# Performance work log

Measured on AMD Instinct MI355X. Metric: run time of the kernel, lower is better.

Reference implementation:

```python
import jax, jax.numpy as jnp
import numpy as np

GRID_LON = 17  # idx = lat*17 + lon in original code


def setup_inputs() -> dict:
    key = jax.random.key(0)
    ks = jax.random.split(key, 16)
    B, S, L = 512, 256, 64
    DIM_RHO, DIM_C, HID = 256, 128, 512
    N_LAT, N_LON = 17, GRID_LON

    rho = jax.random.normal(ks[0], (B, S, DIM_RHO), dtype=jnp.float32)
    c = jax.random.normal(ks[1], (1, DIM_C, N_LAT, N_LON), dtype=jnp.float32)
    w = jax.random.uniform(ks[2], (B, S), dtype=jnp.float32, minval=1e-3, maxval=1.0)
    l = jax.random.uniform(ks[3], (B,), dtype=jnp.float32, minval=0.1, maxval=10.0)
    roads = jax.random.randint(ks[4], (B, L), 0, N_LAT * N_LON)
    lon_idx = jax.random.randint(ks[5], (B, L), 0, N_LON)
    lat_idx = jax.random.randint(ks[6], (B, L), 0, N_LAT)

    sc = lambda fan_in: 1.0 / np.sqrt(fan_in)
    # f2: MLP(128, 256, 128) with selu
    f2_W1 = jax.random.uniform(ks[7], (DIM_C, 256), jnp.float32, -sc(DIM_C), sc(DIM_C))
    f2_b1 = jnp.zeros((256,), jnp.float32)
    f2_W2 = jax.random.uniform(ks[8], (256, DIM_C), jnp.float32, -sc(256), sc(256))
    f2_b2 = jnp.zeros((DIM_C,), jnp.float32)
    # f: MLP2(dim_rho + dim_c, hidden, 1) with selu (use_selu=True)
    fin = DIM_RHO + DIM_C
    f_W1 = jax.random.uniform(ks[9], (fin, HID), jnp.float32, -sc(fin), sc(fin))
    f_b1 = jnp.zeros((HID,), jnp.float32)
    f_W21 = jax.random.uniform(ks[10], (HID, 1), jnp.float32, -sc(HID), sc(HID))
    f_b21 = jnp.zeros((1,), jnp.float32)
    f_W22 = jax.random.uniform(ks[11], (HID, 1), jnp.float32, -sc(HID), sc(HID))
    f_b22 = jnp.zeros((1,), jnp.float32)

    return dict(rho=rho, c=c, w=w, l=l, roads=roads, lon_idx=lon_idx,
                lat_idx=lat_idx, f2_W1=f2_W1, f2_b1=f2_b1, f2_W2=f2_W2,
                f2_b2=f2_b2, f_W1=f_W1, f_b1=f_b1, f_W21=f_W21, f_b21=f_b21,
                f_W22=f_W22, f_b22=f_b22)


def reference(rho, c, w, l, roads, lon_idx, lat_idx,
              f2_W1, f2_b1, f2_W2, f2_b2,
              f_W1, f_b1, f_W21, f_b21, f_W22, f_b22):
    # c: (1, dim_c, n_lat, n_lon) -> (n_lat*n_lon, dim_c)
    c3 = jnp.squeeze(c, 0)                       # (dim_c, n_lat, n_lon)
    c_flat = jnp.transpose(c3, (1, 2, 0)).reshape(-1, c3.shape[0])  # (cells, dim_c)

    # ragged gather-mean, vectorized: (B, L) cell indices -> (B, dim_c)
    idx = lat_idx * GRID_LON + lon_idx           # (B, L)
    c_traj = jnp.mean(c_flat[idx], axis=1)       # (B, dim_c)

    # f2: selu MLP (dropout inactive / eval mode)
    h = jax.nn.selu(c_traj @ f2_W1 + f2_b1)
    c_tr = h @ f2_W2 + f2_b2                     # (B, dim_c)

    # broadcast over seq and concat with rho
    S = rho.shape[1]
    c_exp = jnp.broadcast_to(c_tr[:, None, :], (rho.shape[0], S, c_tr.shape[-1]))
    x = jnp.concatenate([rho, c_exp], axis=2)    # (B, S, dim_rho + dim_c)

    # f (MLP2, selu since use_selu=True)
    h1 = jax.nn.selu(x @ f_W1 + f_b1)            # (B, S, hidden)
    logm = (h1 @ f_W21 + f_b21)[..., 0]          # (B, S)
    logv = (h1 @ f_W22 + f_b22)[..., 0]          # (B, S)

    logw = jnp.log(w)
    logm_agg = jax.nn.logsumexp(logm + logw, axis=1)       # (B,)
    logv_agg = jax.nn.logsumexp(logv + 2.0 * logw, axis=1) # (B,)
    logl = jnp.log(l)
    log_mu = logl - logm_agg
    log_lambda = logl - 3.0 * logm_agg - logv_agg
    return (log_mu, log_lambda)
```

## Files before the change

### kernel.cpp

```cpp
#include <hip/hip_runtime.h>
#include <hip/hip_bf16.h>

typedef short bf16x8 __attribute__((ext_vector_type(8)));
typedef float f32x4 __attribute__((ext_vector_type(4)));
typedef _Float16 half4 __attribute__((ext_vector_type(4)));

__device__ __forceinline__ short f2bf(float f) {
    union { float f; unsigned u; } v; v.f = f;
    unsigned r = (v.u + 0x7FFFu + ((v.u >> 16) & 1u)) >> 16;
    return (short)r;
}

__device__ __forceinline__ float selu_f(float x) {
    const float scale = 1.0507009873554805f;
    const float sa = 1.0507009873554805f * 1.6732632423543772f;
    return x > 0.f ? scale * x : sa * (__expf(x) - 1.f);
}

__global__ void __launch_bounds__(512) prep_all_kernel(
    const float* __restrict__ c, const int* __restrict__ lat_idx,
    const int* __restrict__ lon_idx,
    const float* __restrict__ f2W1, const float* __restrict__ f2b1,
    const float* __restrict__ f2W2, const float* __restrict__ f2b2,
    const float* __restrict__ fW1, const float* __restrict__ fb1,
    const float* __restrict__ fW21, const float* __restrict__ fW22,
    short* __restrict__ w1img, _Float16* __restrict__ wvec,
    float* __restrict__ cbias)
{
    const int bid = blockIdx.x;
    const int t = threadIdx.x;

    if (bid < 512) {
        __shared__ int cells[64];
        __shared__ float ctraj[128];
        __shared__ float hbuf[256];
        __shared__ float ctrf[128];
        const int b = bid;

        if (t < 64) cells[t] = lat_idx[b * 64 + t] * 17 + lon_idx[b * 64 + t];
        __syncthreads();

        if (t < 128) {
            float s = 0.f;
            #pragma unroll 8
            for (int j = 0; j < 64; ++j) s += c[t * 289 + cells[j]];
            ctraj[t] = s * (1.f / 64.f);
        }
        __syncthreads();

        if (t < 256) {
            float acc = f2b1[t];
            #pragma unroll 8
            for (int i = 0; i < 128; ++i) acc += ctraj[i] * f2W1[i * 256 + t];
            hbuf[t] = selu_f(acc);
        }
        __syncthreads();

        if (t < 128) {
            float acc = f2b2[t];
            #pragma unroll 8
            for (int i = 0; i < 256; ++i) acc += hbuf[i] * f2W2[i * 128 + t];
            ctrf[t] = acc;
        }
        __syncthreads();

        float acc = fb1[t];
        #pragma unroll 8
        for (int i = 0; i < 128; ++i) acc += ctrf[i] * fW1[(256 + i) * 512 + t];
        cbias[b * 512 + t] = acc;
    } else if (bid < 768) {
        int I = (bid - 512) * 512 + t;
        int e = I & 7;
        int lane = (I >> 3) & 63;
        int cg = (I >> 9) & 31;
        int kc = I >> 14;
        int col = cg * 16 + (lane & 15);
        int k = kc * 32 + ((lane >> 4) << 3) + e;
        w1img[I] = f2bf(fW1[k * 512 + col]);
    } else {
        int I = (bid - 768) * 512 + t;
        int e = I & 3;
        int lane = (I >> 2) & 63;
        int nc = I >> 8;
        int l15 = lane & 15, hi = lane >> 4;
        int n = nc * 16 + hi * 4 + e;
        float v = (l15 == 0) ? fW21[n] : (l15 == 1 ? fW22[n] : 0.f);
        wvec[I] = (_Float16)v;
    }
}

__global__ void __launch_bounds__(512, 4) fused_gemm_kernel(
    const float* __restrict__ rho, const short* __restrict__ w1img,
    const float* __restrict__ cbias, const _Float16* __restrict__ wvec,
    float* __restrict__ plmP, float* __restrict__ plvP)
{
    __shared__ __align__(16) char smA[36864];

    const int tid  = threadIdx.x;
    const int lane = tid & 63;
    const int w    = tid >> 6;
    const int l15  = lane & 15;
    const int hi   = lane >> 4;

    const int b  = blockIdx.x >> 3;
    const int s0 = ((blockIdx.x >> 1) & 3) << 6;
    const int nh = blockIdx.x & 1;

    const char* bp = (const char*)w1img + (nh * 16 + w * 2) * 1024 + lane * 16;
    bf16x8 bAll[16];
    #pragma unroll
    for (int j = 0; j < 16; ++j)
        bAll[j] = *(const bf16x8*)(bp + (size_t)(j >> 1) * 32768 + (j & 1) * 1024);

    {
        const float* src = rho + (size_t)(b * 256 + s0) * 256 + tid * 8;
        float4 fa[8];
        #pragma unroll
        for (int j = 0; j < 4; ++j) {
            fa[2 * j]     = *(const float4*)(src + j * 4096);
            fa[2 * j + 1] = *(const float4*)(src + j * 4096 + 4);
        }
        const int kc_w = (tid >> 2) & 7;
        const int hi_w = tid & 3;
        const int sw_w = (tid >> 5) ^ (tid & 15);
        #pragma unroll
        for (int j = 0; j < 4; ++j) {
            union { bf16x8 h; unsigned u[4]; } pk;
            asm("v_cvt_pk_bf16_f32 %0, %1, %2" : "=v"(pk.u[0]) : "v"(fa[2*j].x), "v"(fa[2*j].y));
            asm("v_cvt_pk_bf16_f32 %0, %1, %2" : "=v"(pk.u[1]) : "v"(fa[2*j].z), "v"(fa[2*j].w));
            asm("v_cvt_pk_bf16_f32 %0, %1, %2" : "=v"(pk.u[2]) : "v"(fa[2*j+1].x), "v"(fa[2*j+1].y));
            asm("v_cvt_pk_bf16_f32 %0, %1, %2" : "=v"(pk.u[3]) : "v"(fa[2*j+1].z), "v"(fa[2*j+1].w));
            int slot = (kc_w * 4 + j) * 64 + hi_w * 16 + sw_w;
            *(bf16x8*)(smA + (slot << 4)) = pk.h;
        }
    }
    __syncthreads();

    f32x4 acc[2][4];
    #pragma unroll
    for (int nf = 0; nf < 2; ++nf)
        #pragma unroll
        for (int sf = 0; sf < 4; ++sf)
            acc[nf][sf] = (f32x4){0.f, 0.f, 0.f, 0.f};

    #pragma unroll
    for (int kc = 0; kc < 8; ++kc) {
        const int sw_r = l15 ^ (((kc & 3) << 2) | hi);
        const char* ab = smA + ((kc * 256 + hi * 16 + sw_r) << 4);
        bf16x8 aF[4];
        #pragma unroll
        for (int sf = 0; sf < 4; ++sf)
            aF[sf] = *(const bf16x8*)(ab + sf * 1024);
        #pragma unroll
        for (int nf = 0; nf < 2; ++nf)
            #pragma unroll
            for (int sf = 0; sf < 4; ++sf)
                acc[nf][sf] = __builtin_amdgcn_mfma_f32_16x16x32_bf16(
                    bAll[kc * 2 + nf], aF[sf], acc[nf][sf], 0, 0, 0);
    }

    f32x4 rd[4];
    #pragma unroll
    for (int sf = 0; sf < 4; ++sf) rd[sf] = (f32x4){0.f, 0.f, 0.f, 0.f};

    #pragma unroll
    for (int nf = 0; nf < 2; ++nf) {
        const int nc = nh * 16 + w * 2 + nf;
        f32x4 cbf = *(const f32x4*)(cbias + b * 512 + nc * 16 + hi * 4);
        half4 wv = *(const half4*)(wvec + (size_t)nc * 256 + lane * 4);
        #pragma unroll
        for (int sf = 0; sf < 4; ++sf) {
            half4 pa;
            #pragma unroll
            for (int q = 0; q < 4; ++q)
                pa[q] = (_Float16)selu_f(acc[nf][sf][q] + cbf[q]);
            rd[sf] = __builtin_amdgcn_mfma_f32_16x16x16f16(pa, wv, rd[sf], 0, 0, 0);
        }
    }

    float* redM = (float*)(smA + 32768);
    float* redV = (float*)(smA + 34816);
    if (l15 == 0) {
        #pragma unroll
        for (int sf = 0; sf < 4; ++sf)
            *(f32x4*)&redM[w * 64 + sf * 16 + hi * 4] = rd[sf];
    } else if (l15 == 1) {
        #pragma unroll
        for (int sf = 0; sf < 4; ++sf)
            *(f32x4*)&redV[w * 64 + sf * 16 + hi * 4] = rd[sf];
    }

    __syncthreads();
    size_t obase = (size_t)nh * 131072 + (size_t)b * 256 + s0;
    if (tid < 64) {
        float s = 0.f;
        #pragma unroll
        for (int j = 0; j < 8; ++j) s += redM[j * 64 + tid];
        plmP[obase + tid] = s;
    } else if (tid < 128) {
        int rr = tid - 64;
        float s = 0.f;
        #pragma unroll
        for (int j = 0; j < 8; ++j) s += redV[j * 64 + rr];
        plvP[obase + rr] = s;
    }
}

__global__ void __launch_bounds__(64) finalize_kernel(
    const float* __restrict__ plmP, const float* __restrict__ plvP,
    const float* __restrict__ w, const float* __restrict__ l,
    const float* __restrict__ b21p, const float* __restrict__ b22p,
    float* __restrict__ out)
{
    const int b = blockIdx.x;
    const int lane = threadIdx.x;
    const float b21 = b21p[0], b22 = b22p[0];

    float a1[4], a2[4];
    float m1 = -1e30f, m2 = -1e30f;
    #pragma unroll
    for (int i = 0; i < 4; ++i) {
        int s = i * 64 + lane;
        int idx = b * 256 + s;
        float lw = logf(w[idx]);
        a1[i] = plmP[idx] + plmP[131072 + idx] + b21 + lw;
        a2[i] = plvP[idx] + plvP[131072 + idx] + b22 + 2.f * lw;
        m1 = fmaxf(m1, a1[i]);
        m2 = fmaxf(m2, a2[i]);
    }
    #pragma unroll
    for (int m = 1; m < 64; m <<= 1) {
        m1 = fmaxf(m1, __shfl_xor(m1, m));
        m2 = fmaxf(m2, __shfl_xor(m2, m));
    }
    float s1 = 0.f, s2 = 0.f;
    #pragma unroll
    for (int i = 0; i < 4; ++i) {
        s1 += expf(a1[i] - m1);
        s2 += expf(a2[i] - m2);
    }
    #pragma unroll
    for (int m = 1; m < 64; m <<= 1) {
        s1 += __shfl_xor(s1, m);
        s2 += __shfl_xor(s2, m);
    }
    if (lane == 0) {
        float lm_agg = m1 + logf(s1);
        float lv_agg = m2 + logf(s2);
        float logl = logf(l[b]);
        out[b]       = logl - lm_agg;
        out[512 + b] = logl - 3.f * lm_agg - lv_agg;
    }
}

extern "C" void kernel_launch(void* const* d_in, const int* in_sizes, int n_in,
                              void* d_out, int out_size, void* d_ws, size_t ws_size,
                              hipStream_t stream) {
    const float* rho     = (const float*)d_in[0];
    const float* c       = (const float*)d_in[1];
    const float* w       = (const float*)d_in[2];
    const float* l       = (const float*)d_in[3];
    const int*   lon_idx = (const int*)d_in[5];
    const int*   lat_idx = (const int*)d_in[6];
    const float* f2W1    = (const float*)d_in[7];
    const float* f2b1    = (const float*)d_in[8];
    const float* f2W2    = (const float*)d_in[9];
    const float* f2b2    = (const float*)d_in[10];
    const float* fW1     = (const float*)d_in[11];
    const float* fb1     = (const float*)d_in[12];
    const float* fW21    = (const float*)d_in[13];
    const float* fb21    = (const float*)d_in[14];
    const float* fW22    = (const float*)d_in[15];
    const float* fb22    = (const float*)d_in[16];
    float* out = (float*)d_out;

    char* ws = (char*)d_ws;
    float*     cbias = (float*)(ws);
    short*     w1img = (short*)(ws + 1048576);
    float*     plmP  = (float*)(ws + 1310720);
    float*     plvP  = (float*)(ws + 2359296);
    _Float16*  wvec  = (_Float16*)(ws + 3407872);

    prep_all_kernel<<<784, 512, 0, stream>>>(c, lat_idx, lon_idx,
                                             f2W1, f2b1, f2W2, f2b2,
                                             fW1, fb1, fW21, fW22,
                                             w1img, wvec, cbias);
    fused_gemm_kernel<<<4096, 512, 0, stream>>>(rho, w1img, cbias, wvec,
                                                plmP, plvP);
    finalize_kernel<<<512, 64, 0, stream>>>(plmP, plvP, w, l, fb21, fb22, out);
}
```

Measured before the change: 98.66 us.

## Make GEMM blocks persistent over four seq tiles with double-buffered rho staging

Each block now handles all four 64-row sequence tiles for one batch and one N-half, so the grid shrinks from 4096 to 1024 blocks. The bf16 weight fragments are loaded once and reused across the tiles. The next tile's rho loads are issued before the current tile's MFMA work and converted into a second LDS buffer, overlapping global loads with compute. In exchange, LDS use roughly doubles to 68KB, which can lower occupancy, there are fewer blocks to spread across CUs, and register pressure rises from holding the prefetched data.

```diff
diff --git a/kernel.cpp b/kernel.cpp
--- a/kernel.cpp
+++ b/kernel.cpp
@@ -94,7 +94,7 @@
     const float* __restrict__ cbias, const _Float16* __restrict__ wvec,
     float* __restrict__ plmP, float* __restrict__ plvP)
 {
-    __shared__ __align__(16) char smA[36864];
+    __shared__ __align__(16) char smem[69632];
 
     const int tid  = threadIdx.x;
     const int lane = tid & 63;
@@ -102,9 +102,9 @@
     const int l15  = lane & 15;
     const int hi   = lane >> 4;
 
-    const int b  = blockIdx.x >> 3;
-    const int s0 = ((blockIdx.x >> 1) & 3) << 6;
-    const int nh = blockIdx.x & 1;
+    const int bid = blockIdx.x;
+    const int nh  = (bid >> 3) & 1;
+    const int b   = ((bid >> 4) << 3) | (bid & 7);
 
     const char* bp = (const char*)w1img + (nh * 16 + w * 2) * 1024 + lane * 16;
     bf16x8 bAll[16];
@@ -112,97 +112,158 @@
     for (int j = 0; j < 16; ++j)
         bAll[j] = *(const bf16x8*)(bp + (size_t)(j >> 1) * 32768 + (j & 1) * 1024);
 
+    const int kc_w = (tid >> 2) & 7;
+    const int hi_w = tid & 3;
+    const int sw_w = (tid >> 5) ^ (tid & 15);
+    const float* srcB = rho + (size_t)(b * 256) * 256 + tid * 8;
+
+    float* redM = (float*)(smem + 65536);
+    float* redV = (float*)(smem + 67584);
+
     {
-        const float* src = rho + (size_t)(b * 256 + s0) * 256 + tid * 8;
-        float4 fa[8];
         #pragma unroll
         for (int j = 0; j < 4; ++j) {
-            fa[2 * j]     = *(const float4*)(src + j * 4096);
-            fa[2 * j + 1] = *(const float4*)(src + j * 4096 + 4);
-        }
-        const int kc_w = (tid >> 2) & 7;
-        const int hi_w = tid & 3;
-        const int sw_w = (tid >> 5) ^ (tid & 15);
-        #pragma unroll
-        for (int j = 0; j < 4; ++j) {
+            float4 f0 = *(const float4*)(srcB + j * 4096);
+            float4 f1 = *(const float4*)(srcB + j * 4096 + 4);
             union { bf16x8 h; unsigned u[4]; } pk;
-            asm("v_cvt_pk_bf16_f32 %0, %1, %2" : "=v"(pk.u[0]) : "v"(fa[2*j].x), "v"(fa[2*j].y));
-            asm("v_cvt_pk_bf16_f32 %0, %1, %2" : "=v"(pk.u[1]) : "v"(fa[2*j].z), "v"(fa[2*j].w));
-            asm("v_cvt_pk_bf16_f32 %0, %1, %2" : "=v"(pk.u[2]) : "v"(fa[2*j+1].x), "v"(fa[2*j+1].y));
-            asm("v_cvt_pk_bf16_f32 %0, %1, %2" : "=v"(pk.u[3]) : "v"(fa[2*j+1].z), "v"(fa[2*j+1].w));
+            asm("v_cvt_pk_bf16_f32 %0, %1, %2" : "=v"(pk.u[0]) : "v"(f0.x), "v"(f0.y));
+            asm("v_cvt_pk_bf16_f32 %0, %1, %2" : "=v"(pk.u[1]) : "v"(f0.z), "v"(f0.w));
+            asm("v_cvt_pk_bf16_f32 %0, %1, %2" : "=v"(pk.u[2]) : "v"(f1.x), "v"(f1.y));
+            asm("v_cvt_pk_bf16_f32 %0, %1, %2" : "=v"(pk.u[3]) : "v"(f1.z), "v"(f1.w));
             int slot = (kc_w * 4 + j) * 64 + hi_w * 16 + sw_w;
-            *(bf16x8*)(smA + (slot << 4)) = pk.h;
+            *(bf16x8*)(smem + (slot << 4)) = pk.h;
         }
     }
     __syncthreads();
 
-    f32x4 acc[2][4];
-    #pragma unroll
-    for (int nf = 0; nf < 2; ++nf)
-        #pragma unroll
-        for (int sf = 0; sf < 4; ++sf)
-            acc[nf][sf] = (f32x4){0.f, 0.f, 0.f, 0.f};
-
-    #pragma unroll
-    for (int kc = 0; kc < 8; ++kc) {
-        const int sw_r = l15 ^ (((kc & 3) << 2) | hi);
-        const char* ab = smA + ((kc * 256 + hi * 16 + sw_r) << 4);
-        bf16x8 aF[4];
-        #pragma unroll
-        for (int sf = 0; sf < 4; ++sf)
-            aF[sf] = *(const bf16x8*)(ab + sf * 1024);
+    #pragma unroll
+    for (int st = 0; st < 4; ++st) {
+        char* bufC = smem + (st & 1) * 32768;
+        char* bufN = smem + ((st + 1) & 1) * 32768;
+        const float* srcN = srcB + (st + 1) * 16384;
+
+        float4 fa0, fa1, fa2, fa3;
+        if (st < 3) {
+            fa0 = *(const float4*)(srcN);
+            fa1 = *(const float4*)(srcN + 4);
+            fa2 = *(const float4*)(srcN + 4096);
+            fa3 = *(const float4*)(srcN + 4096 + 4);
+        }
+
+        f32x4 acc[2][4];
         #pragma unroll
         for (int nf = 0; nf < 2; ++nf)
             #pragma unroll
             for (int sf = 0; sf < 4; ++sf)
-                acc[nf][sf] = __builtin_amdgcn_mfma_f32_16x16x32_bf16(
-                    bAll[kc * 2 + nf], aF[sf], acc[nf][sf], 0, 0, 0);
-    }
-
-    f32x4 rd[4];
-    #pragma unroll
-    for (int sf = 0; sf < 4; ++sf) rd[sf] = (f32x4){0.f, 0.f, 0.f, 0.f};
-
-    #pragma unroll
-    for (int nf = 0; nf < 2; ++nf) {
-        const int nc = nh * 16 + w * 2 + nf;
-        f32x4 cbf = *(const f32x4*)(cbias + b * 512 + nc * 16 + hi * 4);
-        half4 wv = *(const half4*)(wvec + (size_t)nc * 256 + lane * 4);
-        #pragma unroll
-        for (int sf = 0; sf < 4; ++sf) {
-            half4 pa;
-            #pragma unroll
-            for (int q = 0; q < 4; ++q)
-                pa[q] = (_Float16)selu_f(acc[nf][sf][q] + cbf[q]);
-            rd[sf] = __builtin_amdgcn_mfma_f32_16x16x16f16(pa, wv, rd[sf], 0, 0, 0);
-        }
-    }
-
-    float* redM = (float*)(smA + 32768);
-    float* redV = (float*)(smA + 34816);
-    if (l15 == 0) {
-        #pragma unroll
-        for (int sf = 0; sf < 4; ++sf)
-            *(f32x4*)&redM[w * 64 + sf * 16 + hi * 4] = rd[sf];
-    } else if (l15 == 1) {
-        #pragma unroll
-        for (int sf = 0; sf < 4; ++sf)
-            *(f32x4*)&redV[w * 64 + sf * 16 + hi * 4] = rd[sf];
-    }
-
-    __syncthreads();
-    size_t obase = (size_t)nh * 131072 + (size_t)b * 256 + s0;
-    if (tid < 64) {
-        float s = 0.f;
-        #pragma unroll
-        for (int j = 0; j < 8; ++j) s += redM[j * 64 + tid];
-        plmP[obase + tid] = s;
-    } else if (tid < 128) {
-        int rr = tid - 64;
-        float s = 0.f;
-        #pragma unroll
-        for (int j = 0; j < 8; ++j) s += redV[j * 64 + rr];
-        plvP[obase + rr] = s;
+                acc[nf][sf] = (f32x4){0.f, 0.f, 0.f, 0.f};
+
+        #pragma unroll
+        for (int kc = 0; kc < 8; ++kc) {
+            const int sw_r = l15 ^ (((kc & 3) << 2) | hi);
+            const char* ab = bufC + ((kc * 256 + hi * 16 + sw_r) << 4);
+            bf16x8 aF[4];
+            #pragma unroll
+            for (int sf = 0; sf < 4; ++sf)
+                aF[sf] = *(const bf16x8*)(ab + sf * 1024);
+            #pragma unroll
+            for (int nf = 0; nf < 2; ++nf)
+                #pragma unroll
+                for (int sf = 0; sf < 4; ++sf)
+                    acc[nf][sf] = __builtin_amdgcn_mfma_f32_16x16x32_bf16(
+                        bAll[kc * 2 + nf], aF[sf], acc[nf][sf], 0, 0, 0);
+        }
+
+        float4 fb0, fb1v, fb2, fb3;
+        if (st < 3) {
+            {
+                union { bf16x8 h; unsigned u[4]; } pk;
+                asm("v_cvt_pk_bf16_f32 %0, %1, %2" : "=v"(pk.u[0]) : "v"(fa0.x), "v"(fa0.y));
+                asm("v_cvt_pk_bf16_f32 %0, %1, %2" : "=v"(pk.u[1]) : "v"(fa0.z), "v"(fa0.w));
+                asm("v_cvt_pk_bf16_f32 %0, %1, %2" : "=v"(pk.u[2]) : "v"(fa1.x), "v"(fa1.y));
+                asm("v_cvt_pk_bf16_f32 %0, %1, %2" : "=v"(pk.u[3]) : "v"(fa1.z), "v"(fa1.w));
+                int slot = (kc_w * 4 + 0) * 64 + hi_w * 16 + sw_w;
+                *(bf16x8*)(bufN + (slot << 4)) = pk.h;
+            }
+            {
+                union { bf16x8 h; unsigned u[4]; } pk;
+                asm("v_cvt_pk_bf16_f32 %0, %1, %2" : "=v"(pk.u[0]) : "v"(fa2.x), "v"(fa2.y));
+                asm("v_cvt_pk_bf16_f32 %0, %1, %2" : "=v"(pk.u[1]) : "v"(fa2.z), "v"(fa2.w));
+                asm("v_cvt_pk_bf16_f32 %0, %1, %2" : "=v"(pk.u[2]) : "v"(fa3.x), "v"(fa3.y));
+                asm("v_cvt_pk_bf16_f32 %0, %1, %2" : "=v"(pk.u[3]) : "v"(fa3.z), "v"(fa3.w));
+                int slot = (kc_w * 4 + 1) * 64 + hi_w * 16 + sw_w;
+                *(bf16x8*)(bufN + (slot << 4)) = pk.h;
+            }
+            fb0  = *(const float4*)(srcN + 2 * 4096);
+            fb1v = *(const float4*)(srcN + 2 * 4096 + 4);
+            fb2  = *(const float4*)(srcN + 3 * 4096);
+            fb3  = *(const float4*)(srcN + 3 * 4096 + 4);
+        }
+
+        f32x4 rd[4];
+        #pragma unroll
+        for (int sf = 0; sf < 4; ++sf) rd[sf] = (f32x4){0.f, 0.f, 0.f, 0.f};
+
+        #pragma unroll
+        for (int nf = 0; nf < 2; ++nf) {
+            const int nc = nh * 16 + w * 2 + nf;
+            f32x4 cbf = *(const f32x4*)(cbias + b * 512 + nc * 16 + hi * 4);
+            half4 wv = *(const half4*)(wvec + (size_t)nc * 256 + lane * 4);
+            #pragma unroll
+            for (int sf = 0; sf < 4; ++sf) {
+                half4 pa;
+                #pragma unroll
+                for (int q = 0; q < 4; ++q)
+                    pa[q] = (_Float16)selu_f(acc[nf][sf][q] + cbf[q]);
+                rd[sf] = __builtin_amdgcn_mfma_f32_16x16x16f16(pa, wv, rd[sf], 0, 0, 0);
+            }
+        }
+
+        if (l15 == 0) {
+            #pragma unroll
+            for (int sf = 0; sf < 4; ++sf)
+                *(f32x4*)&redM[w * 64 + sf * 16 + hi * 4] = rd[sf];
+        } else if (l15 == 1) {
+            #pragma unroll
+            for (int sf = 0; sf < 4; ++sf)
+                *(f32x4*)&redV[w * 64 + sf * 16 + hi * 4] = rd[sf];
+        }
+
+        __syncthreads();
+
+        size_t obase = (size_t)nh * 131072 + (size_t)b * 256 + st * 64;
+        if (tid < 64) {
+            float s = 0.f;
+            #pragma unroll
+            for (int j = 0; j < 8; ++j) s += redM[j * 64 + tid];
+            plmP[obase + tid] = s;
+        } else if (tid < 128) {
+            int rr = tid - 64;
+            float s = 0.f;
+            #pragma unroll
+            for (int j = 0; j < 8; ++j) s += redV[j * 64 + rr];
+            plvP[obase + rr] = s;
+        }
+        if (st < 3) {
+            {
+                union { bf16x8 h; unsigned u[4]; } pk;
+                asm("v_cvt_pk_bf16_f32 %0, %1, %2" : "=v"(pk.u[0]) : "v"(fb0.x), "v"(fb0.y));
+                asm("v_cvt_pk_bf16_f32 %0, %1, %2" : "=v"(pk.u[1]) : "v"(fb0.z), "v"(fb0.w));
+                asm("v_cvt_pk_bf16_f32 %0, %1, %2" : "=v"(pk.u[2]) : "v"(fb1v.x), "v"(fb1v.y));
+                asm("v_cvt_pk_bf16_f32 %0, %1, %2" : "=v"(pk.u[3]) : "v"(fb1v.z), "v"(fb1v.w));
+                int slot = (kc_w * 4 + 2) * 64 + hi_w * 16 + sw_w;
+                *(bf16x8*)(bufN + (slot << 4)) = pk.h;
+            }
+            {
+                union { bf16x8 h; unsigned u[4]; } pk;
+                asm("v_cvt_pk_bf16_f32 %0, %1, %2" : "=v"(pk.u[0]) : "v"(fb2.x), "v"(fb2.y));
+                asm("v_cvt_pk_bf16_f32 %0, %1, %2" : "=v"(pk.u[1]) : "v"(fb2.z), "v"(fb2.w));
+                asm("v_cvt_pk_bf16_f32 %0, %1, %2" : "=v"(pk.u[2]) : "v"(fb3.x), "v"(fb3.y));
+                asm("v_cvt_pk_bf16_f32 %0, %1, %2" : "=v"(pk.u[3]) : "v"(fb3.z), "v"(fb3.w));
+                int slot = (kc_w * 4 + 3) * 64 + hi_w * 16 + sw_w;
+                *(bf16x8*)(bufN + (slot << 4)) = pk.h;
+            }
+        }
+        __syncthreads();
     }
 }
 
@@ -285,7 +346,7 @@
                                              f2W1, f2b1, f2W2, f2b2,
                                              fW1, fb1, fW21, fW22,
                                              w1img, wvec, cbias);
-    fused_gemm_kernel<<<4096, 512, 0, stream>>>(rho, w1img, cbias, wvec,
+    fused_gemm_kernel<<<1024, 512, 0, stream>>>(rho, w1img, cbias, wvec,
                                                 plmP, plvP);
     finalize_kernel<<<512, 64, 0, stream>>>(plmP, plvP, w, l, fb21, fb22, out);
 }
```

Measured after the change: 133.6 us. +35.5%, slower.
